# Performance work log

Hardware: AMD Instinct MI355X
Metric: run time of the kernel (lower is better)

Reference implementation:

```python
import jax, jax.numpy as jnp
import numpy as np

MD = 4       # max displacement per level (md=[4,...] in VCN)
WSIZE = 3    # truncation window half-size in flow_reg


def _corrf(ref, tar, md=MD):
    """VCN.corrf: per-channel shifted-product 4D cost volume + leaky_relu.
    cost[b,c,i,j,y,x] = leaky_relu(ref[b,c,y,x] * tar[b,c,y+(j-md), x+(i-md)], 0.1)
    (zero outside valid region, matching the torch zero-filled buffer)."""
    B, C, H, W = ref.shape
    U = 2 * md + 1
    tar_pad = jnp.pad(tar, ((0, 0), (0, 0), (md, md), (md, md)))
    # dim 2 ordered as i*U + j (i = x-shift index, j = y-shift index)
    shifts = jnp.stack([tar_pad[:, :, j:j + H, i:i + W]
                        for i in range(U) for j in range(U)], axis=2)
    cost = jax.nn.leaky_relu(ref[:, :, None] * shifts, 0.1)
    return cost.reshape(B, C, U, U, H, W)


def _flow_reg(x, md=MD, wsize=WSIZE):
    """flow_reg with ent=True: argmax -> 7x7 box mask over (u,v) (the MaxPool3d on a
    one-hot scatter is exactly a Chebyshev-box around the argmax) -> masked softmax
    over u*v -> soft-argmax flow + local/global entropies."""
    B, U, V, H, W = x.shape
    idx = jnp.argmax(x.reshape(B, U * V, H, W), axis=1)         # (B,H,W)
    ub, vb = idx // V, idx % V
    uu = jnp.arange(U)[None, :, None, None, None]
    vv = jnp.arange(V)[None, None, :, None, None]
    mask = (jnp.abs(uu - ub[:, None, None]) <= wsize) & \
           (jnp.abs(vv - vb[:, None, None]) <= wsize)           # (B,U,V,H,W)
    neg_inf = jnp.array(-jnp.inf, x.dtype)
    p = jax.nn.softmax(jnp.where(mask, x, neg_inf).reshape(B, U * V, H, W),
                       axis=1).reshape(B, U, V, H, W)
    fx = (jnp.arange(U) - md).astype(x.dtype)[None, :, None, None, None]
    fy = (jnp.arange(V) - md).astype(x.dtype)[None, None, :, None, None]
    outx = jnp.sum(p * fx, axis=(1, 2))[:, None]                # (B,1,H,W)
    outy = jnp.sum(p * fy, axis=(1, 2))[:, None]
    def _ent(q):
        return (-q * jnp.log(jnp.clip(q, 1e-9, 1 - 1e-9))).sum(axis=(1, 2))[:, None]
    local_ent = _ent(p) / np.log((2 * wsize + 1) ** 2).astype(np.float32)
    pg = jax.nn.softmax(x.reshape(B, U * V, H, W), axis=1).reshape(B, U, V, H, W)
    global_ent = _ent(pg) / np.log(U * V).astype(np.float32)
    return jnp.concatenate([outx, outy], 1), jnp.concatenate([local_ent, global_ent], 1)


def _warp(x, flo):
    """grid_sample-based backward warp (bilinear, zero padding, align_corners=True)
    plus the in-bounds mask, exactly as VCN's warp()."""
    B, C, H, W = x.shape
    px = jnp.arange(W, dtype=flo.dtype)[None, None, :] + flo[:, 0]   # (B,H,W)
    py = jnp.arange(H, dtype=flo.dtype)[None, :, None] + flo[:, 1]
    inb = (jnp.abs(2.0 * px / max(W - 1, 1) - 1.0) < 1) & \
          (jnp.abs(2.0 * py / max(H - 1, 1) - 1.0) < 1)
    x0 = jnp.floor(px); y0 = jnp.floor(py)
    wx = px - x0; wy = py - y0
    x0i = x0.astype(jnp.int32); y0i = y0.astype(jnp.int32)
    flat = x.reshape(B, C, H * W)
    def tap(yi, xi, wgt):
        valid = (xi >= 0) & (xi < W) & (yi >= 0) & (yi < H)
        lin = jnp.clip(yi, 0, H - 1) * W + jnp.clip(xi, 0, W - 1)
        v = jax.vmap(lambda img, l: img[:, l])(flat, lin)            # (B,C,H,W)
        return v * (wgt * valid.astype(x.dtype))[:, None]
    out = (tap(y0i,     x0i,     (1 - wx) * (1 - wy)) +
           tap(y0i,     x0i + 1, wx * (1 - wy)) +
           tap(y0i + 1, x0i,     (1 - wx) * wy) +
           tap(y0i + 1, x0i + 1, wx * wy))
    return out * inb.astype(x.dtype)[:, None], inb


def setup_inputs() -> dict:
    key = jax.random.key(0)
    k1, k2, k3 = jax.random.split(key, 3)
    B, C, H, W, F = 2, 128, 64, 64, 16
    ref = jax.random.normal(k1, (B, C, H, W), jnp.float32) * 0.5
    tar = jax.random.normal(k2, (B, C, H, W), jnp.float32) * 0.5
    pw = jax.random.normal(k3, (F, C), jnp.float32) / np.sqrt(C).astype(np.float32)
    return {"ref_feat": ref, "tar_feat": tar, "proj_w": pw}


def reference(ref_feat, tar_feat, proj_w):
    B, C, H, W = ref_feat.shape
    F_ = proj_w.shape[0]
    U = 2 * MD + 1
    cost = _corrf(ref_feat, tar_feat)                       # (B,C,U,U,H,W)
    # 1x1 channel contraction of the 4D cost volume (butterfly4D input proj)
    cvol = jnp.einsum('bcuvhw,fc->bfuvhw', cost, proj_w)    # (B,F,U,U,H,W)
    flow_h, ent_h = _flow_reg(cvol.reshape(B * F_, U, U, H, W))
    flow = flow_h.reshape(B, F_, 2, H, W)[:, 0]             # first hypothesis
    warped, _ = _warp(tar_feat, flow)
    return jnp.concatenate([flow_h, ent_h], axis=1), warped
```

## Files before the change

kernel.cpp:

```cpp
#include <hip/hip_runtime.h>
#include <math.h>

#define B_ 2
#define C_ 128
#define H_ 64
#define W_ 64
#define F_ 16
#define U_ 9
#define MD_ 4
#define HW_ (H_*W_)
#define BF_ (B_*F_)

typedef float f32x4 __attribute__((ext_vector_type(4)));
typedef float f32x2 __attribute__((ext_vector_type(2)));
typedef _Float16 f16x2 __attribute__((ext_vector_type(2)));
typedef _Float16 f16x4 __attribute__((ext_vector_type(4)));
typedef _Float16 f16x8 __attribute__((ext_vector_type(8)));

#define XSCALE   64.0f
#define WSCALE   256.0f
#define UNSCALE  (1.0f / 16384.0f)

#define TB0  0
#define TB1  7344
#define TSTR 34
#define REFO 14688
#define SM_  5832
#define SI_  6344
#define SU_  6856
#define FX_  9928
#define FY_  9944
#define LDSZ 16800

static __device__ __forceinline__ f16x8 cat4(f16x2 a, f16x2 b, f16x2 c, f16x2 d) {
    f16x4 ab = __builtin_shufflevector(a, b, 0, 1, 2, 3);
    f16x4 cd = __builtin_shufflevector(c, d, 0, 1, 2, 3);
    return __builtin_shufflevector(ab, cd, 0, 1, 2, 3, 4, 5, 6, 7);
}

static __device__ __forceinline__ void split2(f32x2 p, f16x2& hi, f16x2& lo) {
    hi = __builtin_bit_cast(f16x2, __builtin_amdgcn_cvt_pkrtz(p.x, p.y));
    f32x2 hf; hf.x = (float)hi.x; hf.y = (float)hi.y;
    f32x2 l = p - hf;
    lo = __builtin_bit_cast(f16x2, __builtin_amdgcn_cvt_pkrtz(l.x, l.y));
}

__global__ __launch_bounds__(512, 2)
void fused_kernel(const float* __restrict__ ref,
                  const float* __restrict__ tar,
                  const float* __restrict__ pw,
                  float* __restrict__ out0,
                  float* __restrict__ warped) {
    const int t    = threadIdx.x;
    const int lane = t & 63;
    const int wid  = t >> 6;
    const int ml   = lane & 15;
    const int grp  = lane >> 4;

    const int n0 = blockIdx.x;
    const int L  = (n0 & 7) * 64 + (n0 >> 3);
    const int b  = L >> 8;
    const int y  = (L >> 2) & 63;
    const int xq = L & 3;
    const int x0 = xq * 16;

    const int start = wid ? (1 + wid * 10) : 0;

    __shared__ float lds[LDSZ];

    const float* refB = ref + ((size_t)b * C_) * HW_ + y * W_ + x0;
    const float* tarB = tar + ((size_t)b * C_) * HW_;

    int off[11];
    #pragma unroll
    for (int i = 0; i < 11; ++i) {
        int uv = start + i;
        int uu = uv / 9;
        off[i] = ((uv - uu * 9) * 24 + uu) * TSTR;
    }
    const int mlg = ml * TSTR + grp * 8;

    const int sc = t & 31;
    const int sr = t >> 5;
    const bool sact = (t < 288);
    const int ysr  = y + sr - 4;
    const bool sok = sact && ((unsigned)ysr < 64u);
    const int xlo = (xq == 0) ? 0 : (xq == 3 ? 40 : x0 - 4);
    const int sh  = x0 - 4 - xlo;
    const float* tS = tarB + (size_t)sc * HW_ + (sok ? ysr : 0) * W_ + xlo;
    unsigned cmask = 0;
    #pragma unroll
    for (int j = 0; j < 24; ++j)
        if ((unsigned)(x0 - 4 + j) < 64u) cmask |= (1u << j);

    f32x4 g[6];
#define ISSUE(KC) if (sok) {                                                  \
        const float* gp = tS + (size_t)((KC) * 32) * HW_;                     \
        _Pragma("unroll")                                                     \
        for (int q = 0; q < 6; ++q) g[q] = *(const f32x4*)(gp + 4 * q);       \
    }

#define SWR(BUF, S) {                                                         \
        float* dst = lds + (BUF) + (sr * 24) * TSTR + sc;                     \
        _Pragma("unroll")                                                     \
        for (int j = 0; j < 24; ++j) {                                        \
            float v_ = 0.f;                                                   \
            if ((j + (S)) >= 0 && (j + (S)) < 24)                             \
                if ((cmask >> j) & 1u) v_ = g[(j + (S)) >> 2][(j + (S)) & 3]; \
            dst[j * TSTR] = v_;                                               \
        } }

#define SWRITE(KC, BUF) {                                                     \
        if (sok) {                                                            \
            if (sh == 0)     { SWR(BUF, 0) }                                  \
            else if (sh < 0) { SWR(BUF, -4) }                                 \
            else             { SWR(BUF, 4) }                                  \
        } else if (sact && (KC) < 2) {     \
            float* dst = lds + (BUF) + (sr * 24) * TSTR + sc;                 \
            _Pragma("unroll")                                                 \
            for (int j = 0; j < 24; ++j) dst[j * TSTR] = 0.f;                 \
        } }

#define TCOMP(SL, I) {                                                        \
        f16x2 xh4[4], xl4[4];                                                 \
        _Pragma("unroll")                                                     \
        for (int jp = 0; jp < 4; ++jp) {                                      \
            f32x2 p  = rv2[jp] * tv[SL][jp];                                  \
            f32x2 p1 = p * 0.1f;                                              \
            p = __builtin_elementwise_max(p, p1);                             \
            split2(p, xh4[jp], xl4[jp]);                                      \
        }                                                                     \
        f16x8 xhi = cat4(xh4[0], xh4[1], xh4[2], xh4[3]);                     \
        f16x8 xlo = cat4(xl4[0], xl4[1], xl4[2], xl4[3]);                     \
        acc[I] = __builtin_amdgcn_mfma_f32_16x16x32_f16(whi, xhi, acc[I], 0, 0, 0); \
        acc[I] = __builtin_amdgcn_mfma_f32_16x16x32_f16(wlo, xhi, acc[I], 0, 0, 0); \
        acc[I] = __builtin_amdgcn_mfma_f32_16x16x32_f16(whi, xlo, acc[I], 0, 0, 0); }

    f32x4 acc[11];
    #pragma unroll
    for (int i = 0; i < 11; ++i) acc[i] = f32x4{0.f, 0.f, 0.f, 0.f};

    ISSUE(0);
    #pragma unroll
    for (int it = 0; it < 4; ++it) {
        int idx = it * 512 + t;
        int c = idx >> 4, px = idx & 15;
        lds[REFO + px * 132 + c] = refB[(size_t)c * HW_ + px] * XSCALE;
    }
    SWRITE(0, TB0);
    ISSUE(1);
    __syncthreads();

    #pragma unroll
    for (int kc = 0; kc < 4; ++kc) {
        const int tb = (kc & 1) ? TB1 : TB0;

        f32x4 wa = *(const f32x4*)(pw + ml * C_ + kc * 32 + grp * 8);
        f32x4 wb = *(const f32x4*)(pw + ml * C_ + kc * 32 + grp * 8 + 4);
        f16x2 wh[4], wl[4];
        {
            f32x2 p;
            p.x = wa.x * WSCALE; p.y = wa.y * WSCALE; split2(p, wh[0], wl[0]);
            p.x = wa.z * WSCALE; p.y = wa.w * WSCALE; split2(p, wh[1], wl[1]);
            p.x = wb.x * WSCALE; p.y = wb.y * WSCALE; split2(p, wh[2], wl[2]);
            p.x = wb.z * WSCALE; p.y = wb.w * WSCALE; split2(p, wh[3], wl[3]);
        }
        f16x8 whi = cat4(wh[0], wh[1], wh[2], wh[3]);
        f16x8 wlo = cat4(wl[0], wl[1], wl[2], wl[3]);

        f32x4 rva = *(const f32x4*)(lds + REFO + ml * 132 + kc * 32 + grp * 8);
        f32x4 rvb = *(const f32x4*)(lds + REFO + ml * 132 + kc * 32 + grp * 8 + 4);
        f32x2 rv2[4];
        rv2[0].x = rva.x; rv2[0].y = rva.y;
        rv2[1].x = rva.z; rv2[1].y = rva.w;
        rv2[2].x = rvb.x; rv2[2].y = rvb.y;
        rv2[3].x = rvb.z; rv2[3].y = rvb.w;

        f32x2 tv[2][4];
        {
            const float* tp = lds + tb + off[0] + mlg;
            tv[0][0] = *(const f32x2*)(tp);     tv[0][1] = *(const f32x2*)(tp + 2);
            tv[0][2] = *(const f32x2*)(tp + 4); tv[0][3] = *(const f32x2*)(tp + 6);
        }
        #pragma unroll
        for (int i = 0; i < 10; ++i) {
            const int nx = (i + 1) & 1, cu = i & 1;
            const float* tp = lds + tb + off[i + 1] + mlg;
            tv[nx][0] = *(const f32x2*)(tp);     tv[nx][1] = *(const f32x2*)(tp + 2);
            tv[nx][2] = *(const f32x2*)(tp + 4); tv[nx][3] = *(const f32x2*)(tp + 6);
            TCOMP(cu, i);
        }
        if (wid == 0) TCOMP(0, 10);

        if (kc == 0) { SWRITE(1, TB1); ISSUE(2); }
        else if (kc == 1) { SWRITE(2, TB0); ISSUE(3); }
        else if (kc == 2) { SWRITE(3, TB1); }
        __syncthreads();
    }

    int uA[11], vA[11];
    #pragma unroll
    for (int i = 0; i < 11; ++i) {
        int uv = start + i;
        int uu = uv / 9;
        uA[i] = uu; vA[i] = uv - uu * 9;
    }
    const int rem = t & 63;
    const int fl  = rem >> 4;
    const int px  = rem & 15;

    for (int P = 0; P < 4; ++P) {
#define BOUNCE(i) {                                                           \
        if (grp == P) {                                                       \
            int ba = (start + (i)) * 18 + ml;                                 \
            lds[ba        ] = acc[i][0] * UNSCALE;                            \
            lds[ba + 1458 ] = acc[i][1] * UNSCALE;                            \
            lds[ba + 2916 ] = acc[i][2] * UNSCALE;                            \
            lds[ba + 4374 ] = acc[i][3] * UNSCALE; } }
        #pragma unroll
        for (int i = 0; i < 10; ++i) BOUNCE(i);
        if (wid == 0) BOUNCE(10);
        __syncthreads();

        float vv[11];
        #pragma unroll
        for (int i = 0; i < 10; ++i)
            vv[i] = lds[fl * 1458 + (start + i) * 18 + px];
        if (wid == 0) vv[10] = lds[fl * 1458 + 10 * 18 + px];
        float mv = vv[0]; int bi = start;
        #pragma unroll
        for (int i = 1; i < 10; ++i)
            if (vv[i] > mv) { mv = vv[i]; bi = start + i; }
        if (wid == 0 && vv[10] > mv) { mv = vv[10]; bi = 10; }
        lds[SM_ + t] = mv; lds[SI_ + t] = (float)bi;
        __syncthreads();

        float m = lds[SM_ + rem]; int best = (int)lds[SI_ + rem];
        #pragma unroll
        for (int k = 1; k < 8; ++k) {
            float mk = lds[SM_ + k * 64 + rem];
            if (mk > m) { m = mk; best = (int)lds[SI_ + k * 64 + rem]; }
        }
        int ub = best / 9, vb = best - 9 * (best / 9);

        float S = 0.f, A = 0.f, Sx = 0.f, Sy = 0.f, gS = 0.f, gA = 0.f;
#define PH2B(i) {                                                             \
        float d = vv[i] - m; float z = __expf(d);                             \
        gS += z; gA = fmaf(z, d, gA);                                         \
        int duc = uA[i] - ub, dvc = vA[i] - vb;                               \
        bool msk = (duc <= 3) && (duc >= -3) && (dvc <= 3) && (dvc >= -3);    \
        float zm = msk ? z : 0.f, dm = msk ? d : 0.f;                         \
        S += zm; A = fmaf(zm, dm, A);                                         \
        Sx = fmaf(zm, (float)(uA[i] - MD_), Sx);                              \
        Sy = fmaf(zm, (float)(vA[i] - MD_), Sy); }
        #pragma unroll
        for (int i = 0; i < 10; ++i) PH2B(i);
        if (wid == 0) PH2B(10);

        lds[SU_ + 0 * 512 + t] = S;  lds[SU_ + 1 * 512 + t] = A;
        lds[SU_ + 2 * 512 + t] = Sx; lds[SU_ + 3 * 512 + t] = Sy;
        lds[SU_ + 4 * 512 + t] = gS; lds[SU_ + 5 * 512 + t] = gA;
        __syncthreads();

        if (t < 64) {
            float rq[6];
            #pragma unroll
            for (int q = 0; q < 6; ++q) {
                float s = lds[SU_ + q * 512 + t];
                #pragma unroll
                for (int k = 1; k < 8; ++k) s += lds[SU_ + q * 512 + k * 64 + t];
                rq[q] = s;
            }
            float invS = 1.f / rq[0];
            float outx = rq[2] * invS;
            float outy = rq[3] * invS;
            float lent = (logf(rq[0]) - rq[1] * invS) * (1.0f / logf(49.0f));
            float gent = (logf(rq[4]) - rq[5] / rq[4]) * (1.0f / logf(81.0f));
            float* op = out0 + ((size_t)(b * F_ + P * 4 + (t >> 4)) * 4) * HW_
                      + y * W_ + x0 + (t & 15);
            op[0 * HW_] = outx;
            op[1 * HW_] = outy;
            op[2 * HW_] = lent;
            op[3 * HW_] = gent;
            if (P == 0 && t < 16) { lds[FX_ + t] = outx; lds[FY_ + t] = outy; }
        }
    }

    {
        const int pxi = t & 15;
        const int xw  = x0 + pxi;
        float fx = lds[FX_ + pxi], fy = lds[FY_ + pxi];
        float pxw = (float)xw + fx;
        float pyw = (float)y  + fy;
        bool inb = (fabsf(2.0f * pxw / 63.0f - 1.0f) < 1.0f) &&
                   (fabsf(2.0f * pyw / 63.0f - 1.0f) < 1.0f);
        float xf = floorf(pxw), yf = floorf(pyw);
        float wx = pxw - xf, wy = pyw - yf;
        int x0i = (int)xf, y0i = (int)yf;
        auto offn = [&](int yi, int xi, float wgt, float& mw) -> int {
            bool v = ((unsigned)xi < (unsigned)W_) && ((unsigned)yi < (unsigned)H_);
            int xc = xi < 0 ? 0 : (xi > W_ - 1 ? W_ - 1 : xi);
            int yc = yi < 0 ? 0 : (yi > H_ - 1 ? H_ - 1 : yi);
            mw = v ? wgt : 0.f;
            return yc * W_ + xc;
        };
        float m00, m01, m10, m11;
        int o00 = offn(y0i,     x0i,     (1.f - wx) * (1.f - wy), m00);
        int o01 = offn(y0i,     x0i + 1, wx * (1.f - wy),         m01);
        int o10 = offn(y0i + 1, x0i,     (1.f - wx) * wy,         m10);
        int o11 = offn(y0i + 1, x0i + 1, wx * wy,                 m11);
        #pragma unroll
        for (int it = 0; it < 4; ++it) {
            int c = (t >> 4) + 32 * it;
            const float* img = tarB + (size_t)c * HW_;
            float a = img[o00] * m00 + img[o01] * m01
                    + img[o10] * m10 + img[o11] * m11;
            warped[((size_t)(b * C_ + c)) * HW_ + y * W_ + xw] = inb ? a : 0.f;
        }
    }
}

extern "C" void kernel_launch(void* const* d_in, const int* in_sizes, int n_in,
                              void* d_out, int out_size, void* d_ws, size_t ws_size,
                              hipStream_t stream) {
    const float* ref = (const float*)d_in[0];
    const float* tar = (const float*)d_in[1];
    const float* pw  = (const float*)d_in[2];
    float* out0 = (float*)d_out;
    float* out1 = out0 + (size_t)BF_ * 4 * HW_;
    (void)d_ws; (void)ws_size;

    fused_kernel<<<512, 512, 0, stream>>>(ref, tar, pw, out0, out1);
}
```

Measured before the change: 108.2 us.

## Run flow_reg epilogue directly on MFMA accumulator layout, drop per-group LDS bounce

The epilogue no longer copies the MFMA accumulators into LDS in four passes (one per F-group) with a re-read into a pixel-major layout. Each thread now does the argmax, masked softmax and entropy sums in registers on its four accumulator rows, handling all four groups at once. Only the partial max/index and the six sums go through LDS, as f32x4 vectors, and wave 0 reduces them across waves. This cuts the epilogue from about twelve barriers to three and removes scalar LDS traffic, at the cost of more registers held live and a larger LDS footprint for the reduction buffers.

```diff
diff --git a/kernel.cpp b/kernel.cpp
--- a/kernel.cpp
+++ b/kernel.cpp
@@ -25,12 +25,12 @@
 #define TB1  7344
 #define TSTR 34
 #define REFO 14688
-#define SM_  5832
-#define SI_  6344
-#define SU_  6856
-#define FX_  9928
-#define FY_  9944
-#define LDSZ 16800
+#define MXo  0
+#define IXo  2112
+#define SBo  4224
+#define FX_  16896
+#define FY_  16912
+#define LDSZ 16928
 
 static __device__ __forceinline__ f16x8 cat4(f16x2 a, f16x2 b, f16x2 c, f16x2 d) {
     f16x4 ab = __builtin_shufflevector(a, b, 0, 1, 2, 3);
@@ -115,7 +115,7 @@
             if (sh == 0)     { SWR(BUF, 0) }                                  \
             else if (sh < 0) { SWR(BUF, -4) }                                 \
             else             { SWR(BUF, 4) }                                  \
-        } else if (sact && (KC) < 2) {     \
+        } else if (sact && (KC) < 2) {                                        \
             float* dst = lds + (BUF) + (sr * 24) * TSTR + sc;                 \
             _Pragma("unroll")                                                 \
             for (int j = 0; j < 24; ++j) dst[j * TSTR] = 0.f;                 \
@@ -198,6 +198,9 @@
         __syncthreads();
     }
 
+    #pragma unroll
+    for (int i = 0; i < 11; ++i) acc[i] = acc[i] * UNSCALE;
+
     int uA[11], vA[11];
     #pragma unroll
     for (int i = 0; i < 11; ++i) {
@@ -205,86 +208,98 @@
         int uu = uv / 9;
         uA[i] = uu; vA[i] = uv - uu * 9;
     }
-    const int rem = t & 63;
-    const int fl  = rem >> 4;
-    const int px  = rem & 15;
-
-    for (int P = 0; P < 4; ++P) {
-#define BOUNCE(i) {                                                           \
-        if (grp == P) {                                                       \
-            int ba = (start + (i)) * 18 + ml;                                 \
-            lds[ba        ] = acc[i][0] * UNSCALE;                            \
-            lds[ba + 1458 ] = acc[i][1] * UNSCALE;                            \
-            lds[ba + 2916 ] = acc[i][2] * UNSCALE;                            \
-            lds[ba + 4374 ] = acc[i][3] * UNSCALE; } }
-        #pragma unroll
-        for (int i = 0; i < 10; ++i) BOUNCE(i);
-        if (wid == 0) BOUNCE(10);
-        __syncthreads();
-
-        float vv[11];
-        #pragma unroll
-        for (int i = 0; i < 10; ++i)
-            vv[i] = lds[fl * 1458 + (start + i) * 18 + px];
-        if (wid == 0) vv[10] = lds[fl * 1458 + 10 * 18 + px];
-        float mv = vv[0]; int bi = start;
-        #pragma unroll
-        for (int i = 1; i < 10; ++i)
-            if (vv[i] > mv) { mv = vv[i]; bi = start + i; }
-        if (wid == 0 && vv[10] > mv) { mv = vv[10]; bi = 10; }
-        lds[SM_ + t] = mv; lds[SI_ + t] = (float)bi;
-        __syncthreads();
-
-        float m = lds[SM_ + rem]; int best = (int)lds[SI_ + rem];
-        #pragma unroll
-        for (int k = 1; k < 8; ++k) {
-            float mk = lds[SM_ + k * 64 + rem];
-            if (mk > m) { m = mk; best = (int)lds[SI_ + k * 64 + rem]; }
-        }
-        int ub = best / 9, vb = best - 9 * (best / 9);
-
-        float S = 0.f, A = 0.f, Sx = 0.f, Sy = 0.f, gS = 0.f, gA = 0.f;
-#define PH2B(i) {                                                             \
-        float d = vv[i] - m; float z = __expf(d);                             \
-        gS += z; gA = fmaf(z, d, gA);                                         \
-        int duc = uA[i] - ub, dvc = vA[i] - vb;                               \
-        bool msk = (duc <= 3) && (duc >= -3) && (dvc <= 3) && (dvc >= -3);    \
-        float zm = msk ? z : 0.f, dm = msk ? d : 0.f;                         \
-        S += zm; A = fmaf(zm, dm, A);                                         \
-        Sx = fmaf(zm, (float)(uA[i] - MD_), Sx);                              \
-        Sy = fmaf(zm, (float)(vA[i] - MD_), Sy); }
-        #pragma unroll
-        for (int i = 0; i < 10; ++i) PH2B(i);
-        if (wid == 0) PH2B(10);
-
-        lds[SU_ + 0 * 512 + t] = S;  lds[SU_ + 1 * 512 + t] = A;
-        lds[SU_ + 2 * 512 + t] = Sx; lds[SU_ + 3 * 512 + t] = Sy;
-        lds[SU_ + 4 * 512 + t] = gS; lds[SU_ + 5 * 512 + t] = gA;
-        __syncthreads();
-
-        if (t < 64) {
-            float rq[6];
+
+    f32x4 mx = acc[0];
+    f32x4 bix = f32x4{(float)start, (float)start, (float)start, (float)start};
+    #pragma unroll
+    for (int i = 1; i < 10; ++i)
+        #pragma unroll
+        for (int r = 0; r < 4; ++r)
+            if (acc[i][r] > mx[r]) { mx[r] = acc[i][r]; bix[r] = (float)(start + i); }
+    if (wid == 0) {
+        #pragma unroll
+        for (int r = 0; r < 4; ++r)
+            if (acc[10][r] > mx[r]) { mx[r] = acc[10][r]; bix[r] = 10.f; }
+    }
+    *(f32x4*)(lds + MXo + (wid * 4 + grp) * 66 + ml * 4) = mx;
+    *(f32x4*)(lds + IXo + (wid * 4 + grp) * 66 + ml * 4) = bix;
+    __syncthreads();
+
+    f32x4 gm = *(const f32x4*)(lds + MXo + grp * 66 + ml * 4);
+    f32x4 gb = *(const f32x4*)(lds + IXo + grp * 66 + ml * 4);
+    #pragma unroll
+    for (int ch = 1; ch < 8; ++ch) {
+        f32x4 cm = *(const f32x4*)(lds + MXo + (ch * 4 + grp) * 66 + ml * 4);
+        f32x4 cb = *(const f32x4*)(lds + IXo + (ch * 4 + grp) * 66 + ml * 4);
+        #pragma unroll
+        for (int r = 0; r < 4; ++r)
+            if (cm[r] > gm[r]) { gm[r] = cm[r]; gb[r] = cb[r]; }
+    }
+    int ub[4], vb[4];
+    #pragma unroll
+    for (int r = 0; r < 4; ++r) {
+        int bI = (int)gb[r];
+        ub[r] = bI / 9; vb[r] = bI - 9 * ub[r];
+    }
+
+    float S[4]  = {0.f,0.f,0.f,0.f}, Aa[4] = {0.f,0.f,0.f,0.f};
+    float Sx[4] = {0.f,0.f,0.f,0.f}, Sy[4] = {0.f,0.f,0.f,0.f};
+    float gS[4] = {0.f,0.f,0.f,0.f}, gA[4] = {0.f,0.f,0.f,0.f};
+#define PHB(i) {                                                              \
+        _Pragma("unroll")                                                     \
+        for (int r = 0; r < 4; ++r) {                                         \
+            float d = acc[i][r] - gm[r];                                      \
+            float z = __expf(d);                                              \
+            gS[r] += z; gA[r] = fmaf(z, d, gA[r]);                            \
+            int duc = uA[i] - ub[r], dvc = vA[i] - vb[r];                     \
+            bool msk = (duc <= 3) && (duc >= -3) && (dvc <= 3) && (dvc >= -3);\
+            float zm = msk ? z : 0.f, dm = msk ? d : 0.f;                     \
+            S[r] += zm; Aa[r] = fmaf(zm, dm, Aa[r]);                          \
+            Sx[r] = fmaf(zm, (float)(uA[i] - MD_), Sx[r]);                    \
+            Sy[r] = fmaf(zm, (float)(vA[i] - MD_), Sy[r]);                    \
+        } }
+    #pragma unroll
+    for (int i = 0; i < 10; ++i) PHB(i);
+    if (wid == 0) PHB(10);
+
+#define SST(q, a0, a1, a2, a3)                                                \
+    *(f32x4*)(lds + SBo + (((q) * 8 + wid) * 4 + grp) * 66 + ml * 4) =        \
+        f32x4{a0, a1, a2, a3};
+    SST(0, S[0],  S[1],  S[2],  S[3])
+    SST(1, Aa[0], Aa[1], Aa[2], Aa[3])
+    SST(2, Sx[0], Sx[1], Sx[2], Sx[3])
+    SST(3, Sy[0], Sy[1], Sy[2], Sy[3])
+    SST(4, gS[0], gS[1], gS[2], gS[3])
+    SST(5, gA[0], gA[1], gA[2], gA[3])
+    __syncthreads();
+
+    if (wid == 0) {
+        f32x4 rqv[6];
+        #pragma unroll
+        for (int q = 0; q < 6; ++q) {
+            f32x4 s = *(const f32x4*)(lds + SBo + ((q * 8) * 4 + grp) * 66 + ml * 4);
             #pragma unroll
-            for (int q = 0; q < 6; ++q) {
-                float s = lds[SU_ + q * 512 + t];
-                #pragma unroll
-                for (int k = 1; k < 8; ++k) s += lds[SU_ + q * 512 + k * 64 + t];
-                rq[q] = s;
-            }
-            float invS = 1.f / rq[0];
-            float outx = rq[2] * invS;
-            float outy = rq[3] * invS;
-            float lent = (logf(rq[0]) - rq[1] * invS) * (1.0f / logf(49.0f));
-            float gent = (logf(rq[4]) - rq[5] / rq[4]) * (1.0f / logf(81.0f));
-            float* op = out0 + ((size_t)(b * F_ + P * 4 + (t >> 4)) * 4) * HW_
-                      + y * W_ + x0 + (t & 15);
+            for (int ch = 1; ch < 8; ++ch)
+                s += *(const f32x4*)(lds + SBo + ((q * 8 + ch) * 4 + grp) * 66 + ml * 4);
+            rqv[q] = s;
+        }
+        #pragma unroll
+        for (int r = 0; r < 4; ++r) {
+            float invS = 1.f / rqv[0][r];
+            float outx = rqv[2][r] * invS;
+            float outy = rqv[3][r] * invS;
+            float lent = (logf(rqv[0][r]) - rqv[1][r] * invS) * (1.0f / logf(49.0f));
+            float gent = (logf(rqv[4][r]) - rqv[5][r] / rqv[4][r]) * (1.0f / logf(81.0f));
+            float* op = out0 + ((size_t)(b * F_ + grp * 4 + r) * 4) * HW_
+                      + y * W_ + x0 + ml;
             op[0 * HW_] = outx;
             op[1 * HW_] = outy;
             op[2 * HW_] = lent;
             op[3 * HW_] = gent;
-            if (P == 0 && t < 16) { lds[FX_ + t] = outx; lds[FY_ + t] = outy; }
-        }
-    }
+            if (r == 0 && grp == 0) { lds[FX_ + ml] = outx; lds[FY_ + ml] = outy; }
+        }
+    }
+    __syncthreads();
 
     {
         const int pxi = t & 15;
```

Measured after the change: 102.2 us. 5.5% less time.
